# Kernel optimization log

Hardware: AMD Instinct MI355X
Metric: run time of the kernel (lower is better)

The kernel has to match this reference:

```python
import jax, jax.numpy as jnp
import numpy as np

B, S, D, H, E, K, F = 1, 1024, 1024, 16, 8, 2, 4096


def setup_inputs() -> dict:
    key = jax.random.key(0)
    ks = jax.random.split(key, 8)
    n = lambda k, shape, sc: (jax.random.normal(k, shape, dtype=jnp.float32) * sc)
    return {
        "x": n(ks[0], (B, S, D), 1.0),
        "w_qkv": n(ks[1], (D, 3 * D), D ** -0.5),
        "w_o": n(ks[2], (D, D), D ** -0.5),
        "g1": jnp.ones((D,), jnp.float32),
        "b1": jnp.zeros((D,), jnp.float32),
        "wg": n(ks[3], (D, E), D ** -0.5),
        "w1": n(ks[4], (E, D, F), D ** -0.5),
        "bb1": jnp.zeros((E, F), jnp.float32),
        "w2": n(ks[5], (E, F, D), F ** -0.5),
        "bb2": jnp.zeros((E, D), jnp.float32),
        "g2": jnp.ones((D,), jnp.float32),
        "b2": jnp.zeros((D,), jnp.float32),
    }


def layernorm(x, g, b, eps=1e-5):
    m = x.mean(-1, keepdims=True)
    v = ((x - m) ** 2).mean(-1, keepdims=True)
    return (x - m) * jax.lax.rsqrt(v + eps) * g + b


def reference(x, w_qkv, w_o, g1, b1, wg, w1, bb1, w2, bb2, g2, b2):
    b, s, d = x.shape
    hd = d // H
    # --- multi-head causal self-attention ---
    qkv = x @ w_qkv  # [b,s,3d]
    q, k, v = jnp.split(qkv, 3, axis=-1)
    to_heads = lambda t: t.reshape(b, s, H, hd).transpose(0, 2, 1, 3)  # [b,h,s,hd]
    q, k, v = to_heads(q), to_heads(k), to_heads(v)
    scores = jnp.einsum("bhqd,bhkd->bhqk", q, k) / jnp.sqrt(jnp.float32(hd))
    causal = jnp.tril(jnp.ones((s, s), bool))
    scores = jnp.where(causal, scores, jnp.finfo(scores.dtype).min)
    attn = jax.nn.softmax(scores, axis=-1)
    o = jnp.einsum("bhqk,bhkd->bhqd", attn, v)
    o = o.transpose(0, 2, 1, 3).reshape(b, s, d) @ w_o
    # --- add & norm ---
    h = layernorm(x + o, g1, b1)
    # --- MoE FFN: softmax router, top-k, renormalized combine ---
    probs = jax.nn.softmax(h @ wg, axis=-1)  # [b,s,E]
    topv, topi = jax.lax.top_k(probs, K)
    topv = topv / topv.sum(-1, keepdims=True)
    w = (topv[..., None] * jax.nn.one_hot(topi, E, dtype=h.dtype)).sum(-2)  # [b,s,E]
    h1 = jax.nn.gelu(jnp.einsum("bsd,edf->ebsf", h, w1) + bb1[:, None, None, :])
    y = jnp.einsum("ebsf,efd->ebsd", h1, w2) + bb2[:, None, None, :]
    moe = jnp.einsum("ebsd,bse->bsd", y, w)
    # --- residual + norm of MoE block ---
    return layernorm(h + moe, g2, b2)
```

## Files before the change

kernel.cpp:

```cpp
#include <hip/hip_runtime.h>
#include <hip/hip_bf16.h>
#include <math.h>

#define SEQ 1024
#define DIM 1024
#define NH  16
#define NE  8
#define FF  4096
#define NCH 4

typedef float f32x4 __attribute__((ext_vector_type(4)));
typedef float f32x2 __attribute__((ext_vector_type(2)));
typedef short short8 __attribute__((ext_vector_type(8)));
typedef short s16x4 __attribute__((ext_vector_type(4)));

#define WAIT_VM(N) asm volatile("s_waitcnt vmcnt(" #N ")" ::: "memory")

__device__ __forceinline__ ushort f2bf(float f) {
  union { float f; unsigned u; } v; v.f = f;
  unsigned r = v.u + 0x7FFF + ((v.u >> 16) & 1);
  return (ushort)(r >> 16);
}
__device__ __forceinline__ float bf2f(ushort h) {
  union { unsigned u; float f; } v; v.u = ((unsigned)h) << 16;
  return v.f;
}

__device__ __forceinline__ float gelu_tanh(float x) {
  return 0.5f * x * (1.f + tanhf(0.7978845608028654f * (x + 0.044715f * x * x * x)));
}
__device__ __forceinline__ float gelu_fast(float x) {
  float u = 1.5957691216057308f * (x + 0.044715f * x * x * x);
  return x / (1.f + __expf(-u));
}

__device__ __forceinline__ void gl2lds16(const void* g, void* l) {
  __builtin_amdgcn_global_load_lds(
      (const __attribute__((address_space(1))) unsigned int*)g,
      (__attribute__((address_space(3))) unsigned int*)l, 16, 0, 0);
}

__global__ __launch_bounds__(256) void wconv_kernel(
    const float* __restrict__ wq, const float* __restrict__ wo,
    ushort* __restrict__ wqT, ushort* __restrict__ wqTl,
    ushort* __restrict__ woT, ushort* __restrict__ woTl) {
  __shared__ __align__(16) ushort th[64 * 64];
  __shared__ __align__(16) ushort tl[64 * 64];
  int z = blockIdx.z, t = threadIdx.x;
  const float* src; ushort* dh; ushort* dl; int R, C, r0, c0;
  if (z == 0) {
    src = wq; dh = wqT; dl = wqTl;
    R = DIM; C = 3 * DIM; r0 = blockIdx.y * 64; c0 = blockIdx.x * 64;
  } else {
    if (blockIdx.x >= 16) return;
    src = wo; dh = woT; dl = woTl;
    R = DIM; C = DIM; r0 = blockIdx.y * 64; c0 = blockIdx.x * 64;
  }
  int ry = (t >> 4) * 4;
  int cx = (t & 15) * 4;
  f32x4 v[4];
#pragma unroll
  for (int j = 0; j < 4; j++)
    v[j] = *(const f32x4*)&src[(size_t)(r0 + ry + j) * C + c0 + cx];
#pragma unroll
  for (int i = 0; i < 4; i++) {
    int trow = cx + i;
    int o = trow * 64 + (((ry >> 3) ^ (trow & 7)) << 3) + (ry & 7);
    ushort uh[4], ul[4];
#pragma unroll
    for (int j = 0; j < 4; j++) {
      float f = v[j][i];
      ushort hh = f2bf(f);
      uh[j] = hh;
      ul[j] = f2bf(f - bf2f(hh));
    }
    *(s16x4*)&th[o] = *(const s16x4*)uh;
    *(s16x4*)&tl[o] = *(const s16x4*)ul;
  }
  __syncthreads();
  int tr = t >> 2, tc = (t & 3) * 16;
  int b0 = (tc >> 3) ^ (tr & 7);
  int b1 = ((tc >> 3) + 1) ^ (tr & 7);
  size_t dbase = (size_t)(c0 + tr) * R + r0 + tc;
  short8 u0 = *(const short8*)&th[tr * 64 + b0 * 8];
  short8 u1 = *(const short8*)&th[tr * 64 + b1 * 8];
  *(short8*)&dh[dbase] = u0;
  *(short8*)&dh[dbase + 8] = u1;
  short8 l0 = *(const short8*)&tl[tr * 64 + b0 * 8];
  short8 l1 = *(const short8*)&tl[tr * 64 + b1 * 8];
  *(short8*)&dl[dbase] = l0;
  *(short8*)&dl[dbase + 8] = l1;
}

__global__ __launch_bounds__(256) void bfsplit_kernel(const float* __restrict__ in,
                                                      ushort* __restrict__ oh,
                                                      ushort* __restrict__ ol) {
  int i = (blockIdx.x * 256 + threadIdx.x) * 4;
  f32x4 v = *(const f32x4*)&in[i];
  ushort h[4], l[4];
#pragma unroll
  for (int j = 0; j < 4; j++) { h[j] = f2bf(v[j]); l[j] = f2bf(v[j] - bf2f(h[j])); }
  *(s16x4*)&oh[i] = *(const s16x4*)h;
  *(s16x4*)&ol[i] = *(const s16x4*)l;
}

#define MM_FEXP_LOAD(ra0v, ra1v, rb0v, rb1v, rb2v, rb3v, T)            \
  { int _ko = (T) * 32;                                                \
    ra0v = *(const short8*)(aG[0] + _ko);                              \
    ra1v = *(const short8*)(aG[1] + _ko);                              \
    rb0v = *(const f32x4*)(bG + (size_t)(_ko + 0) * N);                \
    rb1v = *(const f32x4*)(bG + (size_t)(_ko + 1) * N);                \
    rb2v = *(const f32x4*)(bG + (size_t)(_ko + 2) * N);                \
    rb3v = *(const f32x4*)(bG + (size_t)(_ko + 3) * N); }

#define MM_FEXP_STAGE(buf, ra0v, ra1v, rb0v, rb1v, rb2v, rb3v)         \
  { *(short8*)&As[buf][aw[0]] = ra0v;                                  \
    *(short8*)&As[buf][aw[1]] = ra1v;                                  \
    _Pragma("unroll")                                                  \
    for (int i = 0; i < 4; i++) {                                      \
      ushort u[4];                                                     \
      u[0] = f2bf(rb0v[i]); u[1] = f2bf(rb1v[i]);                      \
      u[2] = f2bf(rb2v[i]); u[3] = f2bf(rb3v[i]);                      \
      *(s16x4*)&Bs[buf][(nb * 4 + i) * 40 + bslot * 4] = *(const s16x4*)u; } }

#define MM_FEXP_MFMA(buf)                                              \
  { short8 af[4], bf[4];                                               \
    _Pragma("unroll")                                                  \
    for (int mi = 0; mi < 4; mi++) af[mi] = *(const short8*)&As[buf][aro[mi]]; \
    _Pragma("unroll")                                                  \
    for (int ni = 0; ni < 4; ni++) bf[ni] = *(const short8*)&Bs[buf][bro[ni]]; \
    _Pragma("unroll")                                                  \
    for (int mi = 0; mi < 4; mi++)                                     \
      _Pragma("unroll")                                                \
      for (int ni = 0; ni < 4; ni++)                                   \
        acc[mi][ni] = __builtin_amdgcn_mfma_f32_16x16x32_bf16(af[mi], bf[ni], acc[mi][ni], 0, 0, 0); }

template <int EPI, int KSPLIT>
__global__ __launch_bounds__(256) void mm_fexp(
    const ushort* __restrict__ A, const float* __restrict__ Bf,
    const float* __restrict__ bias, void* __restrict__ Cout,
    const int* __restrict__ tok, const int* __restrict__ offcnt,
    int N, int K)
{
  int zz = blockIdx.z;
  int e  = (KSPLIT > 1) ? (zz & (NE - 1)) : zz;
  int ks = (KSPLIT > 1) ? (zz >> 3) : 0;
  int off = offcnt[e], cnt = offcnt[NE + e];
  int m0 = blockIdx.y * 128;
  if (m0 >= cnt) return;
  int n0 = blockIdx.x * 128;
  const float* Bp = Bf + (size_t)e * K * N;
  const int Kc = K / KSPLIT, kbase = ks * Kc;

  __shared__ __align__(16) ushort As[2][128 * 32];
  __shared__ __align__(16) ushort Bs[2][128 * 40];

  int t = threadIdx.x, lane = t & 63, w = t >> 6, wr = w >> 1, wc = w & 1;

  const ushort* aG[2]; int aw[2];
#pragma unroll
  for (int c = 0; c < 2; c++) {
    int gid = w * 128 + c * 64 + lane;
    int m = gid >> 2, p = gid & 3;
    int kg = p ^ ((m >> 1) & 3);
    int mc = m0 + m; if (mc > cnt - 1) mc = cnt - 1;
    int arow = tok ? tok[off + mc] : (off + mc);
    aG[c] = A + (size_t)arow * K + kbase + kg * 8;
    aw[c] = gid * 8;
  }

  int kb = t >> 5, nb = t & 31;
  const float* bG = Bp + (size_t)(kbase + kb * 4) * N + n0 + nb * 4;
  int bslot = kb ^ ((nb & 3) << 1);

  int aro[4], bro[4];
#pragma unroll
  for (int mi = 0; mi < 4; mi++) {
    int m = wr * 64 + mi * 16 + (lane & 15);
    aro[mi] = (m * 4 + ((lane >> 4) ^ ((m >> 1) & 3))) * 8;
  }
#pragma unroll
  for (int ni = 0; ni < 4; ni++) {
    int n = wc * 64 + ni * 16 + (lane & 15);
    bro[ni] = n * 40 + ((((lane >> 4) * 2) ^ (((n >> 2) & 3) << 1))) * 4;
  }

  f32x4 acc[4][4] = {};
  const int nt = Kc / 32;

  short8 raA0, raA1, raB0, raB1;
  f32x4 rbA0, rbA1, rbA2, rbA3, rbB0, rbB1, rbB2, rbB3;
  MM_FEXP_LOAD(raA0, raA1, rbA0, rbA1, rbA2, rbA3, 0);
  MM_FEXP_LOAD(raB0, raB1, rbB0, rbB1, rbB2, rbB3, 1);

  for (int tt = 0; tt < nt; tt += 2) {
    MM_FEXP_STAGE(0, raA0, raA1, rbA0, rbA1, rbA2, rbA3);
    if (tt + 2 < nt) MM_FEXP_LOAD(raA0, raA1, rbA0, rbA1, rbA2, rbA3, tt + 2);
    asm volatile("s_waitcnt lgkmcnt(0)" ::: "memory");
    __builtin_amdgcn_sched_barrier(0);
    __builtin_amdgcn_s_barrier();
    MM_FEXP_MFMA(0);
    MM_FEXP_STAGE(1, raB0, raB1, rbB0, rbB1, rbB2, rbB3);
    if (tt + 3 < nt) MM_FEXP_LOAD(raB0, raB1, rbB0, rbB1, rbB2, rbB3, tt + 3);
    asm volatile("s_waitcnt lgkmcnt(0)" ::: "memory");
    __builtin_amdgcn_sched_barrier(0);
    __builtin_amdgcn_s_barrier();
    MM_FEXP_MFMA(1);
  }

  const float* biasp = (EPI == 3) ? nullptr : bias + (size_t)e * N;
  float* Cp = (float*)Cout + (size_t)ks * 2048 * N;
#pragma unroll
  for (int mi = 0; mi < 4; mi++) {
#pragma unroll
    for (int j = 0; j < 4; j++) {
      int grow = m0 + wr * 64 + mi * 16 + (lane >> 4) * 4 + j;
      if (grow >= cnt) continue;
      size_t rbase = (size_t)(off + grow) * N;
#pragma unroll
      for (int ni = 0; ni < 4; ni++) {
        int gcol = n0 + wc * 64 + ni * 16 + (lane & 15);
        float v = acc[mi][ni][j];
        if (EPI == 1) ((ushort*)Cout)[rbase + gcol] = f2bf(gelu_fast(v + biasp[gcol]));
        else          Cp[rbase + gcol] = v;
      }
    }
  }
}

#undef MM_FEXP_LOAD
#undef MM_FEXP_STAGE
#undef MM_FEXP_MFMA

__global__ __launch_bounds__(256) void mm_split(
    const ushort* __restrict__ Ah, const ushort* __restrict__ Al,
    const ushort* __restrict__ Bh, const ushort* __restrict__ Bl,
    float* __restrict__ C, int N, int K)
{
  int m0 = blockIdx.y * 128;
  int n0 = blockIdx.x * 128;

  __shared__ __align__(16) ushort Ahs[2][4096], Als[2][4096];
  __shared__ __align__(16) ushort Bhs[2][4096], Bls[2][4096];

  int t = threadIdx.x, lane = t & 63, w = t >> 6, wr = w >> 1, wc = w & 1;

  const ushort *aGh[2], *aGl[2], *bGh[2], *bGl[2];
  int lofs[2];
#pragma unroll
  for (int c = 0; c < 2; c++) {
    int gid = w * 128 + c * 64 + lane;
    int m = gid >> 2, p = gid & 3;
    int kg = p ^ ((m >> 1) & 3);
    aGh[c] = Ah + (size_t)(m0 + m) * K + kg * 8;
    aGl[c] = Al + (size_t)(m0 + m) * K + kg * 8;
    bGh[c] = Bh + (size_t)(n0 + m) * K + kg * 8;
    bGl[c] = Bl + (size_t)(n0 + m) * K + kg * 8;
    lofs[c] = (w * 128 + c * 64) * 8;
  }

  int aro[4], bro[4];
#pragma unroll
  for (int mi = 0; mi < 4; mi++) {
    int m = wr * 64 + mi * 16 + (lane & 15);
    aro[mi] = (m * 4 + ((lane >> 4) ^ ((m >> 1) & 3))) * 8;
  }
#pragma unroll
  for (int ni = 0; ni < 4; ni++) {
    int n = wc * 64 + ni * 16 + (lane & 15);
    bro[ni] = (n * 4 + ((lane >> 4) ^ ((n >> 1) & 3))) * 8;
  }

  f32x4 acc[4][4] = {};
  const int nt = K / 32;

#pragma unroll
  for (int c = 0; c < 2; c++) {
    gl2lds16(aGh[c], &Ahs[0][lofs[c]]); gl2lds16(aGl[c], &Als[0][lofs[c]]);
    gl2lds16(bGh[c], &Bhs[0][lofs[c]]); gl2lds16(bGl[c], &Bls[0][lofs[c]]);
  }
  if (nt > 1) {
#pragma unroll
    for (int c = 0; c < 2; c++) {
      gl2lds16(aGh[c] + 32, &Ahs[1][lofs[c]]); gl2lds16(aGl[c] + 32, &Als[1][lofs[c]]);
      gl2lds16(bGh[c] + 32, &Bhs[1][lofs[c]]); gl2lds16(bGl[c] + 32, &Bls[1][lofs[c]]);
    }
  }

  for (int tt = 0; tt < nt; tt++) {
    if (tt + 1 < nt) WAIT_VM(8); else WAIT_VM(0);
    __builtin_amdgcn_s_barrier();
    int b = tt & 1;
    short8 ah[4], al_[4], bh[4], bl_[4];
#pragma unroll
    for (int mi = 0; mi < 4; mi++) {
      ah[mi] = *(const short8*)&Ahs[b][aro[mi]];
      al_[mi] = *(const short8*)&Als[b][aro[mi]];
    }
#pragma unroll
    for (int ni = 0; ni < 4; ni++) {
      bh[ni] = *(const short8*)&Bhs[b][bro[ni]];
      bl_[ni] = *(const short8*)&Bls[b][bro[ni]];
    }
#pragma unroll
    for (int mi = 0; mi < 4; mi++)
#pragma unroll
      for (int ni = 0; ni < 4; ni++) {
        acc[mi][ni] = __builtin_amdgcn_mfma_f32_16x16x32_bf16(al_[mi], bh[ni], acc[mi][ni], 0, 0, 0);
        acc[mi][ni] = __builtin_amdgcn_mfma_f32_16x16x32_bf16(ah[mi], bl_[ni], acc[mi][ni], 0, 0, 0);
        acc[mi][ni] = __builtin_amdgcn_mfma_f32_16x16x32_bf16(ah[mi], bh[ni], acc[mi][ni], 0, 0, 0);
      }
    asm volatile("s_waitcnt lgkmcnt(0)" ::: "memory");
    __builtin_amdgcn_sched_barrier(0);
    __builtin_amdgcn_s_barrier();
    if (tt + 2 < nt) {
      int ko = (tt + 2) * 32;
#pragma unroll
      for (int c = 0; c < 2; c++) {
        gl2lds16(aGh[c] + ko, &Ahs[b][lofs[c]]); gl2lds16(aGl[c] + ko, &Als[b][lofs[c]]);
        gl2lds16(bGh[c] + ko, &Bhs[b][lofs[c]]); gl2lds16(bGl[c] + ko, &Bls[b][lofs[c]]);
      }
    }
  }

#pragma unroll
  for (int mi = 0; mi < 4; mi++)
#pragma unroll
    for (int j = 0; j < 4; j++) {
      int grow = m0 + wr * 64 + mi * 16 + (lane >> 4) * 4 + j;
      size_t rbase = (size_t)grow * N;
#pragma unroll
      for (int ni = 0; ni < 4; ni++) {
        int gcol = n0 + wc * 64 + ni * 16 + (lane & 15);
        C[rbase + gcol] = acc[mi][ni][j];
      }
    }
}

template <int EPI, int SPLIT>
__global__ __launch_bounds__(256) void mm_bf16(
    const float* __restrict__ A, const float* __restrict__ B,
    const float* __restrict__ bias, float* __restrict__ C,
    const int* __restrict__ tok, const int* __restrict__ offcnt,
    int M, int N, int K)
{
  int e = blockIdx.z;
  int off = 0, cnt = M;
  if (offcnt) { off = offcnt[e]; cnt = offcnt[NE + e]; }
  int m0 = blockIdx.y * 128;
  if (m0 >= cnt) return;
  const float* Bp = B + (size_t)e * K * N;
  const float* biasp = (EPI == 0) ? nullptr : bias + (size_t)e * N;
  int n0 = blockIdx.x * 128;

  __shared__ __align__(16) ushort As[(SPLIT + 1) * 128 * 32];
  __shared__ __align__(16) ushort Bs[(SPLIT + 1) * 128 * 32];

  int t = threadIdx.x;
  int lane = t & 63;
  int w = t >> 6, wr = w >> 1, wc = w & 1;

  const float* aptr[2];
  int aws[2];
  for (int i = 0; i < 2; i++) {
    int mr = i * 64 + (t >> 2);
    int mc = m0 + mr; if (mc > cnt - 1) mc = cnt - 1;
    int arow = tok ? tok[off + mc] : (off + mc);
    aptr[i] = A + (size_t)arow * K + (t & 3) * 8;
    aws[i] = mr * 32 + (t & 3) * 8;
  }

  int bn = t >> 1, bkh = (t & 1) * 16;
  const float* bptr = Bp + (size_t)bkh * N + n0 + bn;
  int bws0 = bn * 32 + 8 * (((bkh >> 3) + 0) ^ (bn & 3));
  int bws1 = bn * 32 + 8 * (((bkh >> 3) + 1) ^ (bn & 3));

  int aro[4], bro[4];
#pragma unroll
  for (int mi = 0; mi < 4; mi++)
    aro[mi] = (wr * 64 + mi * 16 + (lane & 15)) * 32 + (lane >> 4) * 8;
#pragma unroll
  for (int ni = 0; ni < 4; ni++) {
    int n = wc * 64 + ni * 16 + (lane & 15);
    bro[ni] = n * 32 + 8 * ((lane >> 4) ^ (n & 3));
  }

  f32x4 acc[4][4] = {};

  for (int k0 = 0; k0 < K; k0 += 32) {
#pragma unroll
    for (int i = 0; i < 2; i++) {
      f32x4 v0 = *(const f32x4*)(aptr[i] + k0);
      f32x4 v1 = *(const f32x4*)(aptr[i] + k0 + 4);
      ushort uh[8], ul[8];
#pragma unroll
      for (int j = 0; j < 4; j++) {
        float f0 = v0[j], f1 = v1[j];
        ushort h0 = f2bf(f0), h1 = f2bf(f1);
        uh[j] = h0; uh[4 + j] = h1;
        if (SPLIT) { ul[j] = f2bf(f0 - bf2f(h0)); ul[4 + j] = f2bf(f1 - bf2f(h1)); }
      }
      *(short8*)&As[aws[i]] = *(const short8*)uh;
      if (SPLIT) *(short8*)&As[4096 + aws[i]] = *(const short8*)ul;
    }
    {
      const float* bp = bptr + (size_t)k0 * N;
      ushort uh[16], ul[16];
#pragma unroll
      for (int i = 0; i < 16; i++) {
        float f = bp[(size_t)i * N];
        ushort h = f2bf(f);
        uh[i] = h;
        if (SPLIT) ul[i] = f2bf(f - bf2f(h));
      }
      *(short8*)&Bs[bws0] = *(const short8*)&uh[0];
      *(short8*)&Bs[bws1] = *(const short8*)&uh[8];
      if (SPLIT) {
        *(short8*)&Bs[4096 + bws0] = *(const short8*)&ul[0];
        *(short8*)&Bs[4096 + bws1] = *(const short8*)&ul[8];
      }
    }
    __syncthreads();
    short8 afh[4], bfh[4], afl[4], bfl[4];
#pragma unroll
    for (int mi = 0; mi < 4; mi++) {
      afh[mi] = *(const short8*)&As[aro[mi]];
      if (SPLIT) afl[mi] = *(const short8*)&As[4096 + aro[mi]];
    }
#pragma unroll
    for (int ni = 0; ni < 4; ni++) {
      bfh[ni] = *(const short8*)&Bs[bro[ni]];
      if (SPLIT) bfl[ni] = *(const short8*)&Bs[4096 + bro[ni]];
    }
#pragma unroll
    for (int mi = 0; mi < 4; mi++)
#pragma unroll
      for (int ni = 0; ni < 4; ni++) {
        if (SPLIT) {
          acc[mi][ni] = __builtin_amdgcn_mfma_f32_16x16x32_bf16(afl[mi], bfh[ni], acc[mi][ni], 0, 0, 0);
          acc[mi][ni] = __builtin_amdgcn_mfma_f32_16x16x32_bf16(afh[mi], bfl[ni], acc[mi][ni], 0, 0, 0);
        }
        acc[mi][ni] = __builtin_amdgcn_mfma_f32_16x16x32_bf16(afh[mi], bfh[ni], acc[mi][ni], 0, 0, 0);
      }
    __syncthreads();
  }

#pragma unroll
  for (int mi = 0; mi < 4; mi++) {
#pragma unroll
    for (int j = 0; j < 4; j++) {
      int grow = m0 + wr * 64 + mi * 16 + (lane >> 4) * 4 + j;
      if (grow >= cnt) continue;
      size_t rbase = (size_t)(off + grow) * N;
#pragma unroll
      for (int ni = 0; ni < 4; ni++) {
        int gcol = n0 + wc * 64 + ni * 16 + (lane & 15);
        float v = acc[mi][ni][j];
        if (EPI >= 1) v += biasp[gcol];
        if (EPI == 1) v = gelu_tanh(v);
        C[rbase + gcol] = v;
      }
    }
  }
}

__device__ __forceinline__ int vidx(int d, int key) {
  return d * 64 + ((((key >> 3) ^ (d & 7)) << 3) | (key & 7));
}

__global__ __launch_bounds__(256, 1) void attn_mfma(const float* __restrict__ qkv,
                                                    float* __restrict__ opart,
                                                    float* __restrict__ ml) {
  const int qb = blockIdx.x;
  const int ch = blockIdx.y;
  const int head = blockIdx.z;
  const int q0 = qb * 128;
  const int t = threadIdx.x;
  const int lane = t & 63, w = t >> 6;
  const int g = lane >> 4, l4 = lane & 15;

  __shared__ __align__(16) ushort Kh[64 * 64], Kl[64 * 64];
  __shared__ __align__(16) ushort Vh[64 * 64], Vl[64 * 64];
  __shared__ __align__(16) ushort Ph[4][32 * 72], Pl[4][32 * 72];

  short8 qh[2][2], ql[2][2];
#pragma unroll
  for (int mi = 0; mi < 2; mi++)
#pragma unroll
    for (int ks = 0; ks < 2; ks++) {
      int row = q0 + w * 32 + mi * 16 + l4;
      const float* qp = qkv + (size_t)row * 3072 + head * 64 + ks * 32 + g * 8;
      f32x4 a = *(const f32x4*)qp;
      f32x4 b4 = *(const f32x4*)(qp + 4);
      ushort uh[8], ul_[8];
#pragma unroll
      for (int j = 0; j < 4; j++) {
        ushort h0 = f2bf(a[j]), h1 = f2bf(b4[j]);
        uh[j] = h0; uh[4 + j] = h1;
        ul_[j] = f2bf(a[j] - bf2f(h0)); ul_[4 + j] = f2bf(b4[j] - bf2f(h1));
      }
      qh[mi][ks] = *(const short8*)uh;
      ql[mi][ks] = *(const short8*)ul_;
    }

  float m_s[2][4], l_s[2][4];
  f32x4 O[2][4] = {};
#pragma unroll
  for (int mi = 0; mi < 2; mi++)
#pragma unroll
    for (int j = 0; j < 4; j++) { m_s[mi][j] = -1e30f; l_s[mi][j] = 0.f; }

  const int ntot = 2 * (qb + 1);
  const int kt_beg = (ch * ntot) / NCH;
  const int kt_end = ((ch + 1) * ntot) / NCH;
  for (int kt = kt_beg; kt < kt_end; kt++) {
    const int kv0 = kt * 64;
    __syncthreads();
    {
      int key = t >> 2;
      int dblk = (t & 3) * 16;
      const float* kp = qkv + (size_t)(kv0 + key) * 3072 + 1024 + head * 64 + dblk;
      const float* vp = kp + 1024;
      f32x4 k0 = *(const f32x4*)kp, k1 = *(const f32x4*)(kp + 4),
            k2 = *(const f32x4*)(kp + 8), k3 = *(const f32x4*)(kp + 12);
      f32x4 v0 = *(const f32x4*)vp, v1 = *(const f32x4*)(vp + 4),
            v2 = *(const f32x4*)(vp + 8), v3 = *(const f32x4*)(vp + 12);
      float kf[16] = {k0[0],k0[1],k0[2],k0[3], k1[0],k1[1],k1[2],k1[3],
                      k2[0],k2[1],k2[2],k2[3], k3[0],k3[1],k3[2],k3[3]};
      float vf[16] = {v0[0],v0[1],v0[2],v0[3], v1[0],v1[1],v1[2],v1[3],
                      v2[0],v2[1],v2[2],v2[3], v3[0],v3[1],v3[2],v3[3]};
#pragma unroll
      for (int half = 0; half < 2; half++) {
        int d8 = (dblk >> 3) + half;
        int idx = key * 64 + ((d8 ^ (key & 7)) << 3);
        ushort uh[8], ul_[8];
#pragma unroll
        for (int j = 0; j < 8; j++) {
          float f = kf[half * 8 + j];
          ushort h = f2bf(f);
          uh[j] = h; ul_[j] = f2bf(f - bf2f(h));
        }
        *(short8*)&Kh[idx] = *(const short8*)uh;
        *(short8*)&Kl[idx] = *(const short8*)ul_;
      }
#pragma unroll
      for (int i = 0; i < 16; i++) {
        int d = dblk + i;
        int idx = vidx(d, key);
        float f = vf[i];
        ushort h = f2bf(f);
        Vh[idx] = h; Vl[idx] = f2bf(f - bf2f(h));
      }
    }
    __syncthreads();

    if (kv0 <= q0 + w * 32 + 31) {
      f32x4 S[2][4] = {};
#pragma unroll
      for (int ks = 0; ks < 2; ks++) {
        short8 kbh[4], kbl[4];
#pragma unroll
        for (int ni = 0; ni < 4; ni++) {
          int key = ni * 16 + l4;
          int d8 = ks * 4 + g;
          int idx = key * 64 + ((d8 ^ (key & 7)) << 3);
          kbh[ni] = *(const short8*)&Kh[idx];
          kbl[ni] = *(const short8*)&Kl[idx];
        }
#pragma unroll
        for (int mi = 0; mi < 2; mi++)
#pragma unroll
          for (int ni = 0; ni < 4; ni++) {
            S[mi][ni] = __builtin_amdgcn_mfma_f32_16x16x32_bf16(ql[mi][ks], kbh[ni], S[mi][ni], 0, 0, 0);
            S[mi][ni] = __builtin_amdgcn_mfma_f32_16x16x32_bf16(qh[mi][ks], kbl[ni], S[mi][ni], 0, 0, 0);
            S[mi][ni] = __builtin_amdgcn_mfma_f32_16x16x32_bf16(qh[mi][ks], kbh[ni], S[mi][ni], 0, 0, 0);
          }
      }
#pragma unroll
      for (int mi = 0; mi < 2; mi++) {
        int rowb = q0 + w * 32 + mi * 16 + g * 4;
        float mx[4] = {-1e30f, -1e30f, -1e30f, -1e30f};
#pragma unroll
        for (int ni = 0; ni < 4; ni++) {
          int col = kv0 + ni * 16 + l4;
#pragma unroll
          for (int j = 0; j < 4; j++) {
            float s = S[mi][ni][j] * 0.125f;
            if (col > rowb + j) s = -1e30f;
            S[mi][ni][j] = s;
            mx[j] = fmaxf(mx[j], s);
          }
        }
#pragma unroll
        for (int j = 0; j < 4; j++) {
#pragma unroll
          for (int msk = 8; msk; msk >>= 1) mx[j] = fmaxf(mx[j], __shfl_xor(mx[j], msk));
          float mn = fmaxf(m_s[mi][j], mx[j]);
          float sc = __expf(m_s[mi][j] - mn);
          m_s[mi][j] = mn;
          l_s[mi][j] *= sc;
#pragma unroll
          for (int df = 0; df < 4; df++) O[mi][df][j] *= sc;
        }
        float ps[4] = {0.f, 0.f, 0.f, 0.f};
#pragma unroll
        for (int ni = 0; ni < 4; ni++)
#pragma unroll
          for (int j = 0; j < 4; j++) {
            float p = __expf(S[mi][ni][j] - m_s[mi][j]);
            ps[j] += p;
            int rl = mi * 16 + g * 4 + j, cl = ni * 16 + l4;
            ushort h = f2bf(p);
            Ph[w][rl * 72 + cl] = h;
            Pl[w][rl * 72 + cl] = f2bf(p - bf2f(h));
          }
#pragma unroll
        for (int j = 0; j < 4; j++) {
#pragma unroll
          for (int msk = 8; msk; msk >>= 1) ps[j] += __shfl_xor(ps[j], msk);
          l_s[mi][j] += ps[j];
        }
      }
      asm volatile("s_waitcnt lgkmcnt(0)" ::: "memory");
      __builtin_amdgcn_sched_barrier(0);
#pragma unroll
      for (int ks = 0; ks < 2; ks++) {
        short8 pah[2], pal[2], vbh[4], vbl[4];
#pragma unroll
        for (int mi = 0; mi < 2; mi++) {
          int idx = (mi * 16 + l4) * 72 + ks * 32 + g * 8;
          pah[mi] = *(const short8*)&Ph[w][idx];
          pal[mi] = *(const short8*)&Pl[w][idx];
        }
#pragma unroll
        for (int df = 0; df < 4; df++) {
          int d = df * 16 + l4;
          int k8 = ks * 4 + g;
          int idx = d * 64 + ((k8 ^ (d & 7)) << 3);
          vbh[df] = *(const short8*)&Vh[idx];
          vbl[df] = *(const short8*)&Vl[idx];
        }
#pragma unroll
        for (int mi = 0; mi < 2; mi++)
#pragma unroll
          for (int df = 0; df < 4; df++) {
            O[mi][df] = __builtin_amdgcn_mfma_f32_16x16x32_bf16(pal[mi], vbh[df], O[mi][df], 0, 0, 0);
            O[mi][df] = __builtin_amdgcn_mfma_f32_16x16x32_bf16(pah[mi], vbl[df], O[mi][df], 0, 0, 0);
            O[mi][df] = __builtin_amdgcn_mfma_f32_16x16x32_bf16(pah[mi], vbh[df], O[mi][df], 0, 0, 0);
          }
      }
    }
  }

#pragma unroll
  for (int mi = 0; mi < 2; mi++)
#pragma unroll
    for (int j = 0; j < 4; j++) {
      int row = q0 + w * 32 + mi * 16 + g * 4 + j;
      if (l4 == 0) {
        float* mlp = ml + (((size_t)ch * NH + head) * SEQ + row) * 2;
        mlp[0] = m_s[mi][j];
        mlp[1] = l_s[mi][j];
      }
#pragma unroll
      for (int df = 0; df < 4; df++)
        opart[(size_t)ch * (SEQ * DIM) + (size_t)row * DIM + head * 64 + df * 16 + l4] =
            O[mi][df][j];
    }
}

template <int SPLIT>
__global__ __launch_bounds__(256) void attn_combine(const float* __restrict__ opart,
                                                    const float* __restrict__ ml,
                                                    float* __restrict__ o,
                                                    ushort* __restrict__ oh,
                                                    ushort* __restrict__ ol) {
  int row = blockIdx.x, t = threadIdx.x;
  int d0 = t * 4;
  int head = d0 >> 6;
  float m[NCH], l[NCH];
#pragma unroll
  for (int ch = 0; ch < NCH; ch++) {
    const float* p = ml + (((size_t)ch * NH + head) * SEQ + row) * 2;
    m[ch] = p[0]; l[ch] = p[1];
  }
  float M = m[0];
#pragma unroll
  for (int ch = 1; ch < NCH; ch++) M = fmaxf(M, m[ch]);
  float wgt[NCH], den = 0.f;
#pragma unroll
  for (int ch = 0; ch < NCH; ch++) { wgt[ch] = __expf(m[ch] - M); den += l[ch] * wgt[ch]; }
  float inv = 1.f / den;
  f32x4 r = {0.f, 0.f, 0.f, 0.f};
#pragma unroll
  for (int ch = 0; ch < NCH; ch++) {
    f32x4 O = *(const f32x4*)&opart[(size_t)ch * (SEQ * DIM) + (size_t)row * DIM + d0];
#pragma unroll
    for (int j = 0; j < 4; j++) r[j] += O[j] * wgt[ch];
  }
#pragma unroll
  for (int j = 0; j < 4; j++) r[j] *= inv;
  if (SPLIT) {
    ushort hh[4], ll[4];
#pragma unroll
    for (int j = 0; j < 4; j++) { hh[j] = f2bf(r[j]); ll[j] = f2bf(r[j] - bf2f(hh[j])); }
    *(s16x4*)&oh[(size_t)row * DIM + d0] = *(const s16x4*)hh;
    *(s16x4*)&ol[(size_t)row * DIM + d0] = *(const s16x4*)ll;
  } else {
    *(f32x4*)&o[(size_t)row * DIM + d0] = r;
  }
}

__device__ float block_reduce_256(float v, float* red, int t) {
  red[t] = v; __syncthreads();
  for (int st = 128; st > 0; st >>= 1) {
    if (t < st) red[t] += red[t + st];
    __syncthreads();
  }
  float r = red[0];
  __syncthreads();
  return r;
}

__global__ __launch_bounds__(256) void addln_router_kernel(
    const float* __restrict__ x, const float* __restrict__ r,
    const float* __restrict__ g, const float* __restrict__ b,
    const float* __restrict__ wg,
    float* __restrict__ out, ushort* __restrict__ outb,
    int* __restrict__ topi, float* __restrict__ topw) {
  __shared__ float red[256];
  __shared__ float red2[NE][256];
  int row = blockIdx.x, t = threadIdx.x;
  float vals[4];
  float s = 0.f;
  for (int i = 0; i < 4; i++) {
    int d = t + i * 256;
    vals[i] = x[(size_t)row * DIM + d] + r[(size_t)row * DIM + d];
    s += vals[i];
  }
  float mean = block_reduce_256(s, red, t) * (1.f / DIM);
  float vs = 0.f;
  for (int i = 0; i < 4; i++) { float d = vals[i] - mean; vs += d * d; }
  float var = block_reduce_256(vs, red, t) * (1.f / DIM);
  float inv = rsqrtf(var + 1e-5f);
  float hv4[4];
  for (int i = 0; i < 4; i++) {
    int d = t + i * 256;
    float v = (vals[i] - mean) * inv * g[d] + b[d];
    hv4[i] = v;
    out[(size_t)row * DIM + d] = v;
    outb[(size_t)row * DIM + d] = f2bf(v);
  }
  float acc[NE] = {};
  for (int i = 0; i < 4; i++) {
    int d = t + i * 256;
    const float* wr = wg + (size_t)d * NE;
    for (int e = 0; e < NE; e++) acc[e] += hv4[i] * wr[e];
  }
  for (int e = 0; e < NE; e++) red2[e][t] = acc[e];
  __syncthreads();
  for (int st = 128; st > 0; st >>= 1) {
    if (t < st)
      for (int e = 0; e < NE; e++) red2[e][t] += red2[e][t + st];
    __syncthreads();
  }
  if (t == 0) {
    float l[NE];
    for (int e = 0; e < NE; e++) l[e] = red2[e][0];
    int i0 = 0;
    for (int e = 1; e < NE; e++) if (l[e] > l[i0]) i0 = e;
    int i1 = -1;
    for (int e = 0; e < NE; e++) {
      if (e == i0) continue;
      if (i1 < 0 || l[e] > l[i1]) i1 = e;
    }
    float p1 = __expf(l[i1] - l[i0]);
    float iv = 1.f / (1.f + p1);
    topi[row * 2] = i0; topi[row * 2 + 1] = i1;
    topw[row * 2] = iv; topw[row * 2 + 1] = p1 * iv;
  }
}

__global__ __launch_bounds__(256) void addln_kernel(const float* __restrict__ x,
                                                    const float* __restrict__ r,
                                                    const float* __restrict__ g,
                                                    const float* __restrict__ b,
                                                    float* __restrict__ out,
                                                    ushort* __restrict__ outb) {
  __shared__ float red[256];
  int row = blockIdx.x, t = threadIdx.x;
  float vals[4];
  float s = 0.f;
  for (int i = 0; i < 4; i++) {
    int d = t + i * 256;
    vals[i] = x[(size_t)row * DIM + d] + r[(size_t)row * DIM + d];
    s += vals[i];
  }
  float mean = block_reduce_256(s, red, t) * (1.f / DIM);
  float vs = 0.f;
  for (int i = 0; i < 4; i++) { float d = vals[i] - mean; vs += d * d; }
  float var = block_reduce_256(vs, red, t) * (1.f / DIM);
  float inv = rsqrtf(var + 1e-5f);
  for (int i = 0; i < 4; i++) {
    int d = t + i * 256;
    float v = (vals[i] - mean) * inv * g[d] + b[d];
    out[(size_t)row * DIM + d] = v;
    if (outb) outb[(size_t)row * DIM + d] = f2bf(v);
  }
}

__global__ __launch_bounds__(256) void router_kernel(const float* __restrict__ h,
                                                     const float* __restrict__ wg,
                                                     int* __restrict__ topi,
                                                     float* __restrict__ topw) {
  __shared__ float red[NE][256];
  int tkn = blockIdx.x, t = threadIdx.x;
  float acc[NE] = {};
  for (int i = 0; i < 4; i++) {
    int d = t + i * 256;
    float hv = h[(size_t)tkn * DIM + d];
    const float* wr = wg + (size_t)d * NE;
    for (int e = 0; e < NE; e++) acc[e] += hv * wr[e];
  }
  for (int e = 0; e < NE; e++) red[e][t] = acc[e];
  __syncthreads();
  for (int st = 128; st > 0; st >>= 1) {
    if (t < st)
      for (int e = 0; e < NE; e++) red[e][t] += red[e][t + st];
    __syncthreads();
  }
  if (t == 0) {
    float l[NE];
    for (int e = 0; e < NE; e++) l[e] = red[e][0];
    int i0 = 0;
    for (int e = 1; e < NE; e++) if (l[e] > l[i0]) i0 = e;
    int i1 = -1;
    for (int e = 0; e < NE; e++) {
      if (e == i0) continue;
      if (i1 < 0 || l[e] > l[i1]) i1 = e;
    }
    float p1 = __expf(l[i1] - l[i0]);
    float inv = 1.f / (1.f + p1);
    topi[tkn * 2] = i0; topi[tkn * 2 + 1] = i1;
    topw[tkn * 2] = inv; topw[tkn * 2 + 1] = p1 * inv;
  }
}

__global__ __launch_bounds__(1024) void compact_kernel(const int* __restrict__ topi,
                                                       int* __restrict__ tok,
                                                       int* __restrict__ assign_row,
                                                       int* __restrict__ offcnt) {
  __shared__ int scan[1024];
  __shared__ int sbase;
  int t = threadIdx.x;
  if (t == 0) sbase = 0;
  __syncthreads();
  for (int e = 0; e < NE; e++) {
    int which = -1;
    if (topi[t * 2] == e) which = 0;
    else if (topi[t * 2 + 1] == e) which = 1;
    scan[t] = (which >= 0) ? 1 : 0;
    __syncthreads();
    for (int s2 = 1; s2 < 1024; s2 <<= 1) {
      int add = (t >= s2) ? scan[t - s2] : 0;
      __syncthreads();
      scan[t] += add;
      __syncthreads();
    }
    int incl = scan[t];
    int total = scan[1023];
    int base = sbase;
    if (which >= 0) {
      int pos = base + incl - 1;
      tok[pos] = t;
      assign_row[t * 2 + which] = pos;
    }
    if (t == 0) { offcnt[e] = base; offcnt[NE + e] = total; }
    __syncthreads();
    if (t == 0) sbase = base + total;
    __syncthreads();
  }
}

template <int KS>
__global__ __launch_bounds__(256) void final_ln_kernel(const float* __restrict__ h,
                                                       const float* __restrict__ y,
                                                       const int* __restrict__ assign_row,
                                                       const float* __restrict__ topw,
                                                       const int* __restrict__ topi,
                                                       const float* __restrict__ bb2,
                                                       const float* __restrict__ g,
                                                       const float* __restrict__ b,
                                                       float* __restrict__ out) {
  __shared__ float red[256];
  int row = blockIdx.x, t = threadIdx.x;
  int r0 = assign_row[row * 2], r1 = assign_row[row * 2 + 1];
  float w0 = topw[row * 2], w1 = topw[row * 2 + 1];
  float vals[4];
  float s = 0.f;
  for (int i = 0; i < 4; i++) {
    int d = t + i * 256;
    float acc0 = 0.f, acc1 = 0.f;
#pragma unroll
    for (int p = 0; p < KS; p++) {
      acc0 += y[(size_t)p * 2048 * DIM + (size_t)r0 * DIM + d];
      acc1 += y[(size_t)p * 2048 * DIM + (size_t)r1 * DIM + d];
    }
    float v = h[(size_t)row * DIM + d] + w0 * acc0 + w1 * acc1;
    if (KS > 1) {
      int e0 = topi[row * 2], e1 = topi[row * 2 + 1];
      v += w0 * bb2[e0 * DIM + d] + w1 * bb2[e1 * DIM + d];
    }
    vals[i] = v;
    s += v;
  }
  float mean = block_reduce_256(s, red, t) * (1.f / DIM);
  float vs = 0.f;
  for (int i = 0; i < 4; i++) { float d = vals[i] - mean; vs += d * d; }
  float var = block_reduce_256(vs, red, t) * (1.f / DIM);
  float inv = rsqrtf(var + 1e-5f);
  for (int i = 0; i < 4; i++) {
    int d = t + i * 256;
    out[(size_t)row * DIM + d] = (vals[i] - mean) * inv * g[d] + b[d];
  }
}

extern "C" void kernel_launch(void* const* d_in, const int* in_sizes, int n_in,
                              void* d_out, int out_size, void* d_ws, size_t ws_size,
                              hipStream_t stream) {
  const float* x     = (const float*)d_in[0];
  const float* w_qkv = (const float*)d_in[1];
  const float* w_o   = (const float*)d_in[2];
  const float* g1    = (const float*)d_in[3];
  const float* b1    = (const float*)d_in[4];
  const float* wg    = (const float*)d_in[5];
  const float* w1    = (const float*)d_in[6];
  const float* bb1   = (const float*)d_in[7];
  const float* w2    = (const float*)d_in[8];
  const float* bb2   = (const float*)d_in[9];
  const float* g2    = (const float*)d_in[10];
  const float* b2    = (const float*)d_in[11];
  float* out = (float*)d_out;
  float* ws = (float*)d_ws;

  const bool fast = ws_size >= (size_t)46671872 * 4;

  if (fast) {
    float* qkv    = ws;
    float* oproj  = ws + 4194304;
    float* h      = ws + 5242880;
    float* ybuf   = ws + 6291456;
    float* topw   = ws + 8388608;
    int*   ibase  = (int*)(ws + 8390656);
    int* topi       = ibase;
    int* tok        = ibase + 2048;
    int* assign_row = ibase + 4096;
    int* offcnt     = ibase + 6144;
    ushort* hb  = (ushort*)(ws + 8398848);
    ushort* h1b = (ushort*)(ws + 8923136);
    ushort* wqT  = (ushort*)(ws + 13117440);
    ushort* wqTl = wqT + 3145728;
    ushort* woT  = wqT + 6291456;
    ushort* woTl = wqT + 7340032;
    float* ypart = ws + 17311744;
    ushort* xh = (ushort*)ybuf;
    ushort* xl = xh + 1048576;
    ushort* oh = xh + 2097152;
    ushort* ol = xh + 3145728;
    float* opart = ypart;
    float* mlbuf = ypart + NCH * 1048576;

    wconv_kernel<<<dim3(48, 16, 2), 256, 0, stream>>>(w_qkv, w_o,
                                                      wqT, wqTl, woT, woTl);
    bfsplit_kernel<<<dim3(SEQ * DIM / 1024), 256, 0, stream>>>(x, xh, xl);
    mm_split<<<dim3(24, 8), 256, 0, stream>>>(xh, xl, wqT, wqTl, qkv, 3 * DIM, DIM);
    attn_mfma<<<dim3(8, NCH, NH), 256, 0, stream>>>(qkv, opart, mlbuf);
    attn_combine<1><<<dim3(SEQ), 256, 0, stream>>>(opart, mlbuf, nullptr, oh, ol);
    mm_split<<<dim3(8, 8), 256, 0, stream>>>(oh, ol, woT, woTl, oproj, DIM, DIM);
    addln_router_kernel<<<dim3(SEQ), 256, 0, stream>>>(x, oproj, g1, b1, wg,
                                                       h, hb, topi, topw);
    compact_kernel<<<dim3(1), 1024, 0, stream>>>(topi, tok, assign_row, offcnt);
    mm_fexp<1, 1><<<dim3(FF / 128, 8, NE), 256, 0, stream>>>(hb, w1, bb1, (void*)h1b,
                                                             tok, offcnt, FF, DIM);
    mm_fexp<3, 4><<<dim3(DIM / 128, 8, NE * 4), 256, 0, stream>>>(h1b, w2, nullptr,
                                                                  (void*)ypart,
                                                                  nullptr, offcnt, DIM, FF);
    final_ln_kernel<4><<<dim3(SEQ), 256, 0, stream>>>(h, ypart, assign_row, topw,
                                                      topi, bb2, g2, b2, out);
  } else {
    float* qkv    = ws;
    float* attn_o = ws + 3145728;
    float* oproj  = ws + 4194304;
    float* h      = ws + 5242880;
    float* h1     = ws + 6291456;
    float* ybuf   = ws + 14680064;
    float* topw   = ws + 16777216;
    int*   ibase  = (int*)(ws + 16779264);
    int* topi       = ibase;
    int* tok        = ibase + 2048;
    int* assign_row = ibase + 4096;
    int* offcnt     = ibase + 6144;
    float* opart = h1;
    float* mlbuf = h1 + NCH * 1048576;

    mm_bf16<0, 1><<<dim3(24, 8, 1), 256, 0, stream>>>(x, w_qkv, nullptr, qkv,
                                                      nullptr, nullptr, SEQ, 3 * DIM, DIM);
    attn_mfma<<<dim3(8, NCH, NH), 256, 0, stream>>>(qkv, opart, mlbuf);
    attn_combine<0><<<dim3(SEQ), 256, 0, stream>>>(opart, mlbuf, attn_o, nullptr, nullptr);
    mm_bf16<0, 1><<<dim3(8, 8, 1), 256, 0, stream>>>(attn_o, w_o, nullptr, oproj,
                                                     nullptr, nullptr, SEQ, DIM, DIM);
    addln_kernel<<<dim3(SEQ), 256, 0, stream>>>(x, oproj, g1, b1, h, nullptr);
    router_kernel<<<dim3(SEQ), 256, 0, stream>>>(h, wg, topi, topw);
    compact_kernel<<<dim3(1), 1024, 0, stream>>>(topi, tok, assign_row, offcnt);
    mm_bf16<1, 0><<<dim3(32, 8, NE), 256, 0, stream>>>(h, w1, bb1, h1,
                                                       tok, offcnt, SEQ, FF, DIM);
    mm_bf16<2, 0><<<dim3(8, 8, NE), 256, 0, stream>>>(h1, w2, bb2, ybuf,
                                                      nullptr, offcnt, SEQ, DIM, FF);
    final_ln_kernel<1><<<dim3(SEQ), 256, 0, stream>>>(h, ybuf, assign_row, topw,
                                                      nullptr, nullptr, g2, b2, out);
  }
}
```

Measured before the change: 312.7 us.

## Fuse x split into weight conversion, use ballot scan, double attention chunks

Three separate changes. The bf16 hi/lo split of x now runs as an extra z-slice of the weight-conversion kernel, which saves one launch. The compaction kernel swaps its log-step shared-memory scan for a wave ballot/popcount scan, which needs far fewer barriers. The attention split-K chunk count NCH goes from 4 to 8 for more parallelism, so the partial buffers and the ml buffer are relocated to fit, at the cost of more partial output to combine.

```diff
diff --git a/kernel.cpp b/kernel.cpp
--- a/kernel.cpp
+++ b/kernel.cpp
@@ -7,7 +7,7 @@
 #define NH  16
 #define NE  8
 #define FF  4096
-#define NCH 4
+#define NCH 8
 
 typedef float f32x4 __attribute__((ext_vector_type(4)));
 typedef float f32x2 __attribute__((ext_vector_type(2)));
@@ -42,13 +42,27 @@
 
 __global__ __launch_bounds__(256) void wconv_kernel(
     const float* __restrict__ wq, const float* __restrict__ wo,
+    const float* __restrict__ x,
     ushort* __restrict__ wqT, ushort* __restrict__ wqTl,
-    ushort* __restrict__ woT, ushort* __restrict__ woTl) {
+    ushort* __restrict__ woT, ushort* __restrict__ woTl,
+    ushort* __restrict__ xh, ushort* __restrict__ xl) {
   __shared__ __align__(16) ushort th[64 * 64];
   __shared__ __align__(16) ushort tl[64 * 64];
   int z = blockIdx.z, t = threadIdx.x;
+  if (z == 2) {
+    int blk = blockIdx.y * 64 + blockIdx.x;
+    int i = (blk * 256 + t) * 4;
+    f32x4 v = *(const f32x4*)&x[i];
+    ushort h[4], l[4];
+#pragma unroll
+    for (int j = 0; j < 4; j++) { h[j] = f2bf(v[j]); l[j] = f2bf(v[j] - bf2f(h[j])); }
+    *(s16x4*)&xh[i] = *(const s16x4*)h;
+    *(s16x4*)&xl[i] = *(const s16x4*)l;
+    return;
+  }
   const float* src; ushort* dh; ushort* dl; int R, C, r0, c0;
   if (z == 0) {
+    if (blockIdx.x >= 48) return;
     src = wq; dh = wqT; dl = wqTl;
     R = DIM; C = 3 * DIM; r0 = blockIdx.y * 64; c0 = blockIdx.x * 64;
   } else {
@@ -850,34 +864,26 @@
                                                        int* __restrict__ tok,
                                                        int* __restrict__ assign_row,
                                                        int* __restrict__ offcnt) {
-  __shared__ int scan[1024];
-  __shared__ int sbase;
-  int t = threadIdx.x;
-  if (t == 0) sbase = 0;
-  __syncthreads();
+  __shared__ int wsum[16];
+  int t = threadIdx.x, lane = t & 63, w = t >> 6;
+  int i0 = topi[t * 2], i1 = topi[t * 2 + 1];
+  int base = 0;
   for (int e = 0; e < NE; e++) {
-    int which = -1;
-    if (topi[t * 2] == e) which = 0;
-    else if (topi[t * 2 + 1] == e) which = 1;
-    scan[t] = (which >= 0) ? 1 : 0;
+    int which = (i0 == e) ? 0 : ((i1 == e) ? 1 : -1);
+    unsigned long long mask = __ballot(which >= 0);
+    unsigned long long lem = (lane == 63) ? ~0ULL : ((1ULL << (lane + 1)) - 1ULL);
+    int incl = __popcll(mask & lem);
+    if (lane == 0) wsum[w] = __popcll(mask);
     __syncthreads();
-    for (int s2 = 1; s2 < 1024; s2 <<= 1) {
-      int add = (t >= s2) ? scan[t - s2] : 0;
-      __syncthreads();
-      scan[t] += add;
-      __syncthreads();
-    }
-    int incl = scan[t];
-    int total = scan[1023];
-    int base = sbase;
+    int pre = 0, tot = 0;
+    for (int i = 0; i < 16; i++) { if (i < w) pre += wsum[i]; tot += wsum[i]; }
     if (which >= 0) {
-      int pos = base + incl - 1;
+      int pos = base + pre + incl - 1;
       tok[pos] = t;
       assign_row[t * 2 + which] = pos;
     }
-    if (t == 0) { offcnt[e] = base; offcnt[NE + e] = total; }
-    __syncthreads();
-    if (t == 0) sbase = base + total;
+    if (t == 0) { offcnt[e] = base; offcnt[NE + e] = tot; }
+    base += tot;
     __syncthreads();
   }
 }
@@ -963,16 +969,15 @@
     ushort* woT  = wqT + 6291456;
     ushort* woTl = wqT + 7340032;
     float* ypart = ws + 17311744;
+    float* mlbuf = ws + 25700352;
     ushort* xh = (ushort*)ybuf;
     ushort* xl = xh + 1048576;
     ushort* oh = xh + 2097152;
     ushort* ol = xh + 3145728;
     float* opart = ypart;
-    float* mlbuf = ypart + NCH * 1048576;
-
-    wconv_kernel<<<dim3(48, 16, 2), 256, 0, stream>>>(w_qkv, w_o,
-                                                      wqT, wqTl, woT, woTl);
-    bfsplit_kernel<<<dim3(SEQ * DIM / 1024), 256, 0, stream>>>(x, xh, xl);
+
+    wconv_kernel<<<dim3(64, 16, 3), 256, 0, stream>>>(w_qkv, w_o, x,
+                                                      wqT, wqTl, woT, woTl, xh, xl);
     mm_split<<<dim3(24, 8), 256, 0, stream>>>(xh, xl, wqT, wqTl, qkv, 3 * DIM, DIM);
     attn_mfma<<<dim3(8, NCH, NH), 256, 0, stream>>>(qkv, opart, mlbuf);
     attn_combine<1><<<dim3(SEQ), 256, 0, stream>>>(opart, mlbuf, nullptr, oh, ol);
@@ -1001,7 +1006,7 @@
     int* assign_row = ibase + 4096;
     int* offcnt     = ibase + 6144;
     float* opart = h1;
-    float* mlbuf = h1 + NCH * 1048576;
+    float* mlbuf = ybuf;
 
     mm_bf16<0, 1><<<dim3(24, 8, 1), 256, 0, stream>>>(x, w_qkv, nullptr, qkv,
                                                       nullptr, nullptr, SEQ, 3 * DIM, DIM);
```

After: 311.6 us, median of 2. No clear change (-0.3%).
